# Kernel tuning notes

Hardware: AMD Instinct MI355X
Metric: run time of the kernel (lower is better)

Reference implementation:

```python
import jax, jax.numpy as jnp
import numpy as np

B = 131072          # batch (x in torch code; t=1, groups=1)
D = 128             # embedding_dim
K = 1024            # num_embeddings (codebook size)
COMMITMENT_COST = 0.25


def setup_inputs() -> dict:
    key = jax.random.key(0)
    k1, k2, k3 = jax.random.split(key, 3)
    inputs = jax.random.normal(k1, (B, D), dtype=jnp.float32)
    embedding = jax.random.normal(k2, (K, D), dtype=jnp.float32)
    # positive EMA cluster sizes (post-warmup state; torch init is zeros)
    ema_cluster_size = jax.random.uniform(k3, (K,), dtype=jnp.float32)
    return {"inputs": inputs, "embedding": embedding,
            "ema_cluster_size": ema_cluster_size}


def reference(inputs, embedding, ema_cluster_size):
    # groups=1, t=1: flat_input == inputs, shape [B, D]
    flat = inputs
    distances = (jnp.sum(flat * flat, axis=1, keepdims=True)
                 + jnp.sum(embedding * embedding, axis=1)
                 - 2.0 * jnp.matmul(flat, embedding.T))
    # module weights distances by EMA cluster size before argmin
    distances = distances * ema_cluster_size[None, :]
    encoding_indices = jnp.argmin(distances, axis=1)            # [B]
    # one-hot @ embedding == gather of codebook rows (same math, efficient)
    quantized = jnp.take(embedding, encoding_indices, axis=0)   # [B, D]
    # commitment loss: mse(stop_grad(quantized), inputs)
    e_latent_loss = jnp.mean((jax.lax.stop_gradient(quantized) - flat) ** 2)
    loss = COMMITMENT_COST * e_latent_loss
    # straight-through estimator
    quantized = flat + jax.lax.stop_gradient(quantized - flat)
    # z_embed: [bs, m] since t=1, groups=1; indices: [bs, groups] = [B, 1]
    z_embed = quantized
    return z_embed, loss, encoding_indices[:, None]
```

## Files before the change

kernel.cpp:

```cpp
#include <hip/hip_runtime.h>

#define DD   128
#define KTOT 1024
#define BTOT 131072

typedef __attribute__((ext_vector_type(8))) short bfrag8;
typedef __attribute__((ext_vector_type(16))) float facc16;

__device__ __forceinline__ unsigned short bf16_rne(float x) {
    unsigned u = __builtin_bit_cast(unsigned, x);
    u += 0x7fffu + ((u >> 16) & 1u);
    return (unsigned short)(u >> 16);
}
__device__ __forceinline__ float bf16f(unsigned short h) {
    unsigned u = ((unsigned)h) << 16;
    return __builtin_bit_cast(float, u);
}
__device__ __forceinline__ void gload_lds16(const void* g, void* l) {
    __builtin_amdgcn_global_load_lds(
        (const __attribute__((address_space(1))) void*)g,
        (__attribute__((address_space(3))) void*)l, 16, 0, 0);
}

__global__ __launch_bounds__(256) void vq_prep(
    const float* __restrict__ E, const float* __restrict__ ema,
    unsigned* __restrict__ Eh32, unsigned* __restrict__ El32,
    float* __restrict__ alpha, float* __restrict__ beta)
{
    const int tid = threadIdx.x, lane = tid & 63, wid = tid >> 6;
    const int k = blockIdx.x * 4 + wid;
    const float2 e2 = *(const float2*)(E + (size_t)k * DD + lane * 2);
    double ss = (double)e2.x * e2.x + (double)e2.y * e2.y;
    #pragma unroll
    for (int off = 1; off < 64; off <<= 1) ss += __shfl_xor(ss, off);
    float w = ema[k];
    float tw = -2.0f * w;
    float v0 = tw * e2.x, v1 = tw * e2.y;
    unsigned short h0 = bf16_rne(v0), h1 = bf16_rne(v1);
    unsigned short l0 = bf16_rne(v0 - bf16f(h0)), l1 = bf16_rne(v1 - bf16f(h1));
    Eh32[k * 64 + lane] = (unsigned)h0 | ((unsigned)h1 << 16);
    El32[k * 64 + lane] = (unsigned)l0 | ((unsigned)l1 << 16);
    if (lane == 0) { alpha[k] = w; beta[k] = (float)((double)w * ss); }
}

__global__ __launch_bounds__(256, 2) void vq_mfma(
    const float* __restrict__ X, const float* __restrict__ E,
    const unsigned short* __restrict__ Eh, const unsigned short* __restrict__ El,
    const float* __restrict__ alpha, const float* __restrict__ beta,
    float* __restrict__ outZ, float* __restrict__ outIdx,
    double* __restrict__ lossAcc, int* __restrict__ refCount,
    int* __restrict__ refList, int refCap)
{
    __shared__ __align__(1024) char smem[33280];
    int* ldsIdx = (int*)(smem + 32768);

    const int tid = threadIdx.x, lane = tid & 63, wid = tid >> 6;
    const int col = lane & 31, g2 = lane >> 5, m15 = lane & 15;
    const int rb = blockIdx.x * 128 + wid * 32;

    int soff[2], dofs[2];
    #pragma unroll
    for (int q = 0; q < 2; ++q) {
        int cb = wid * 8 + q * 4;
        int c = cb + (lane >> 4);
        soff[q] = c * 256 + ((m15 ^ (c & 15)) << 4);
        dofs[q] = cb * 256;
    }
    const char* EhB = (const char*)Eh;
    const char* ElB = (const char*)El;

    #pragma unroll
    for (int q = 0; q < 2; ++q) {
        gload_lds16(EhB + soff[q], smem + dofs[q]);
        gload_lds16(ElB + soff[q], smem + 8192 + dofs[q]);
    }

    bfrag8 Ah[8], Al[8];
    float p = 0.f;
    const float* xr = X + (size_t)(rb + col) * DD + g2 * 8;
    #pragma unroll
    for (int s = 0; s < 8; ++s) {
        float4 v0 = *(const float4*)(xr + s * 16);
        float4 v1 = *(const float4*)(xr + s * 16 + 4);
        float xs8[8] = {v0.x, v0.y, v0.z, v0.w, v1.x, v1.y, v1.z, v1.w};
        #pragma unroll
        for (int j = 0; j < 8; ++j) {
            float x = xs8[j];
            p = fmaf(x, x, p);
            unsigned short h = bf16_rne(x);
            Ah[s][j] = (short)h;
            Al[s][j] = (short)bf16_rne(x - bf16f(h));
        }
    }
    p += __shfl_xor(p, 32);
    float crs[16];
    #pragma unroll
    for (int r = 0; r < 16; ++r)
        crs[r] = __shfl(p, (r & 3) + 8 * (r >> 2) + 4 * g2);

    int rof[8];
    #pragma unroll
    for (int s = 0; s < 8; ++s)
        rof[s] = col * 256 + ((((s << 1) | g2) ^ m15) << 4);

    float b1[16], b2[16];
    int   i1[16];
    #pragma unroll
    for (int r = 0; r < 16; ++r) { b1[r] = 3e38f; b2[r] = 3e38f; i1[r] = 0; }

    __syncthreads();

    int cur = 0;
    #pragma unroll 2
    for (int t = 0; t < 32; ++t) {
        if (t + 1 < 32) {
            const char* eh2 = EhB + (size_t)(t + 1) * 8192;
            const char* el2 = ElB + (size_t)(t + 1) * 8192;
            char* nb = smem + ((cur ^ 1) * 16384);
            #pragma unroll
            for (int q = 0; q < 2; ++q) {
                gload_lds16(eh2 + soff[q], nb + dofs[q]);
                gload_lds16(el2 + soff[q], nb + 8192 + dofs[q]);
            }
        }
        const int cb32 = t * 32;
        float av = alpha[cb32 + col], bv = beta[cb32 + col];
        facc16 acc0, acc1;
        #pragma unroll
        for (int r = 0; r < 16; ++r) { acc0[r] = fmaf(av, crs[r], bv); acc1[r] = 0.f; }

        const char* bb = smem + cur * 16384;
        #pragma unroll
        for (int s = 0; s < 8; ++s) {
            bfrag8 Bh = *(const bfrag8*)(bb + rof[s]);
            bfrag8 Bl = *(const bfrag8*)(bb + 8192 + rof[s]);
            acc0 = __builtin_amdgcn_mfma_f32_32x32x16_bf16(Ah[s], Bh, acc0, 0, 0, 0);
            acc1 = __builtin_amdgcn_mfma_f32_32x32x16_bf16(Ah[s], Bl, acc1, 0, 0, 0);
            acc1 = __builtin_amdgcn_mfma_f32_32x32x16_bf16(Al[s], Bh, acc1, 0, 0, 0);
        }

        #pragma unroll
        for (int r = 0; r < 16; ++r) {
            float dd = acc0[r] + acc1[r];
            bool lt = dd < b1[r];
            b2[r] = fminf(b2[r], fmaxf(b1[r], dd));
            b1[r] = fminf(b1[r], dd);
            i1[r] = lt ? cb32 : i1[r];
        }
        __syncthreads();
        cur ^= 1;
    }

    int code[16];
    #pragma unroll
    for (int r = 0; r < 16; ++r) code[r] = i1[r] + col;
    #pragma unroll
    for (int off = 1; off < 32; off <<= 1) {
        #pragma unroll
        for (int r = 0; r < 16; ++r) {
            float ob1 = __shfl_xor(b1[r], off);
            float ob2 = __shfl_xor(b2[r], off);
            int   oc  = __shfl_xor(code[r], off);
            bool better = (ob1 < b1[r]) || (ob1 == b1[r] && oc < code[r]);
            float nb2 = better ? fminf(ob2, b1[r]) : fminf(b2[r], ob1);
            b1[r]   = better ? ob1 : b1[r];
            code[r] = better ? oc  : code[r];
            b2[r]   = nb2;
        }
    }

    double lsum = 0.0;
    if (col == 0) {
        #pragma unroll
        for (int r = 0; r < 16; ++r) {
            int rl = (r & 3) + 8 * (r >> 2) + 4 * g2;
            int row = rb + rl;
            int bc = code[r];
            outIdx[row] = (float)bc;
            ldsIdx[wid * 32 + rl] = bc;
            lsum += (double)b1[r] / (double)alpha[bc];
            float thr = fmaf(4e-4f, b1[r], 2e-6f);
            if (b2[r] - b1[r] < thr) {
                int pz = atomicAdd(refCount, 1);
                if (pz < refCap) refList[pz] = row;
            }
        }
    }
    lsum += __shfl_xor(lsum, 32);
    if (lane == 0) atomicAdd(lossAcc, lsum);

    __syncthreads();

    {
        int rl = lane >> 1;
        int best = ldsIdx[wid * 32 + rl];
        const float4* src = (const float4*)(E + (size_t)best * DD + (lane & 1) * 64);
        float4* dst = (float4*)(outZ + (size_t)(rb + rl) * DD + (lane & 1) * 64);
        #pragma unroll
        for (int q = 0; q < 16; ++q) dst[q] = src[q];
    }
}

__global__ void vq_refine(const float* __restrict__ X, const float* __restrict__ E,
                          const float* __restrict__ ema,
                          float* __restrict__ outZ, float* __restrict__ outIdx,
                          double* __restrict__ lossAcc,
                          const int* __restrict__ refCount,
                          const int* __restrict__ refList, int refCap)
{
    __shared__ float xs[DD];
    __shared__ double rb[256];
    __shared__ int    ri[256];
    __shared__ int    s_new, s_old;
    const int tid = threadIdx.x;
    int total = *refCount;
    if (total > refCap) total = refCap;

    for (int it = blockIdx.x; it < total; it += gridDim.x) {
        int row = refList[it];
        __syncthreads();
        if (tid < DD) xs[tid] = X[(size_t)row * DD + tid];
        __syncthreads();

        double lb = 1e300; int li = KTOT;
        #pragma unroll
        for (int j = 0; j < KTOT / 256; ++j) {
            int k = tid + j * 256;
            const float* e = E + (size_t)k * DD;
            double s = 0.0;
            for (int d = 0; d < DD; ++d) {
                double t = (double)xs[d] - (double)e[d];
                s = fma(t, t, s);
            }
            s *= (double)ema[k];
            if (s < lb) { lb = s; li = k; }
        }
        rb[tid] = lb; ri[tid] = li;
        __syncthreads();
        for (int st = 128; st > 0; st >>= 1) {
            if (tid < st) {
                double ob = rb[tid + st]; int oi = ri[tid + st];
                if (ob < rb[tid] || (ob == rb[tid] && oi < ri[tid])) { rb[tid] = ob; ri[tid] = oi; }
            }
            __syncthreads();
        }
        if (tid == 0) {
            int ni = ri[0];
            int oi = (int)outIdx[row];
            s_new = ni; s_old = oi;
            if (ni != oi) {
                const float* en = E + (size_t)ni * DD;
                const float* eo = E + (size_t)oi * DD;
                double dl = 0.0;
                for (int d = 0; d < DD; ++d) {
                    double dn  = (double)en[d] - (double)xs[d];
                    double dod = (double)eo[d] - (double)xs[d];
                    dl += dn * dn - dod * dod;
                }
                atomicAdd(lossAcc, dl);
                outIdx[row] = (float)ni;
            }
        }
        __syncthreads();
        if (s_new != s_old && tid < DD)
            outZ[(size_t)row * DD + tid] = E[(size_t)s_new * DD + tid];
    }
}

__global__ void vq_finalize(const double* __restrict__ lossAcc, float* __restrict__ outLoss) {
    *outLoss = (float)(0.25 * (*lossAcc) / ((double)BTOT * (double)DD));
}

extern "C" void kernel_launch(void* const* d_in, const int* in_sizes, int n_in,
                              void* d_out, int out_size, void* d_ws, size_t ws_size,
                              hipStream_t stream)
{
    const float* X   = (const float*)d_in[0];
    const float* E   = (const float*)d_in[1];
    const float* ema = (const float*)d_in[2];

    float* out     = (float*)d_out;
    float* outZ    = out;
    float* outLoss = out + (size_t)BTOT * DD;
    float* outIdx  = outLoss + 1;

    char* ws = (char*)d_ws;
    double* lossAcc = (double*)ws;
    int* refCount   = (int*)(ws + 8);
    float* alpha    = (float*)(ws + 16);
    float* beta     = (float*)(ws + 16 + 4096);
    unsigned short* Eh = (unsigned short*)(ws + 8208);
    unsigned short* El = (unsigned short*)(ws + 270352);
    int* refList    = (int*)(ws + 532496);
    long cap = ((long)ws_size - 532496) / 4;
    if (cap < 0) cap = 0;
    if (cap > BTOT) cap = BTOT;

    hipMemsetAsync(d_ws, 0, 16, stream);
    vq_prep<<<dim3(KTOT / 4), dim3(256), 0, stream>>>(
        E, ema, (unsigned*)Eh, (unsigned*)El, alpha, beta);
    vq_mfma<<<dim3(BTOT / 128), dim3(256), 0, stream>>>(
        X, E, Eh, El, alpha, beta, outZ, outIdx, lossAcc, refCount, refList, (int)cap);
    vq_refine<<<dim3(256), dim3(256), 0, stream>>>(
        X, E, ema, outZ, outIdx, lossAcc, refCount, refList, (int)cap);
    vq_finalize<<<dim3(1), dim3(1), 0, stream>>>(lossAcc, outLoss);
}
```

Measured before the change: 276.1 us.

## Triple-buffer codebook tiles with 512-thread blocks and LDS-cached alpha/beta

The main MFMA kernel now runs 512-thread blocks covering 256 rows, so each staged codebook tile is shared by twice as many waves. Codebook loads into LDS go through a three-stage ring with prefetch distance two. Explicit vmcnt waits and a single barrier per iteration replace the old double buffer, which needed two syncs per tile. Alpha and beta are copied into LDS once per block instead of being read from global memory each tile. The cost is more LDS per block (about 57KB) and register pressure under launch_bounds(512,4), which may limit occupancy or cause spills.

New measurement: 468.3 us. +69.6%, slower.

```diff
diff --git a/kernel.cpp b/kernel.cpp
--- a/kernel.cpp
+++ b/kernel.cpp
@@ -3,6 +3,7 @@
 #define DD   128
 #define KTOT 1024
 #define BTOT 131072
+#define NT   32
 
 typedef __attribute__((ext_vector_type(8))) short bfrag8;
 typedef __attribute__((ext_vector_type(16))) float facc16;
@@ -21,6 +22,7 @@
         (const __attribute__((address_space(1))) void*)g,
         (__attribute__((address_space(3))) void*)l, 16, 0, 0);
 }
+#define WAITV(N) asm volatile("s_waitcnt vmcnt(" #N ")" ::: "memory")
 
 __global__ __launch_bounds__(256) void vq_prep(
     const float* __restrict__ E, const float* __restrict__ ema,
@@ -43,7 +45,7 @@
     if (lane == 0) { alpha[k] = w; beta[k] = (float)((double)w * ss); }
 }
 
-__global__ __launch_bounds__(256, 2) void vq_mfma(
+__global__ __launch_bounds__(512, 4) void vq_mfma(
     const float* __restrict__ X, const float* __restrict__ E,
     const unsigned short* __restrict__ Eh, const unsigned short* __restrict__ El,
     const float* __restrict__ alpha, const float* __restrict__ beta,
@@ -51,28 +53,26 @@
     double* __restrict__ lossAcc, int* __restrict__ refCount,
     int* __restrict__ refList, int refCap)
 {
-    __shared__ __align__(1024) char smem[33280];
-    int* ldsIdx = (int*)(smem + 32768);
+    __shared__ __align__(1024) char smem[58368];
+    float* alphaLds = (float*)(smem + 49152);
+    float* betaLds  = (float*)(smem + 53248);
+    int*   ldsIdx   = (int*)(smem + 57344);
 
     const int tid = threadIdx.x, lane = tid & 63, wid = tid >> 6;
     const int col = lane & 31, g2 = lane >> 5, m15 = lane & 15;
-    const int rb = blockIdx.x * 128 + wid * 32;
-
-    int soff[2], dofs[2];
-    #pragma unroll
-    for (int q = 0; q < 2; ++q) {
-        int cb = wid * 8 + q * 4;
-        int c = cb + (lane >> 4);
-        soff[q] = c * 256 + ((m15 ^ (c & 15)) << 4);
-        dofs[q] = cb * 256;
-    }
+    const int rb = blockIdx.x * 256 + wid * 32;
+
+    const int c0 = tid >> 4;
+    const int soff = c0 * 256 + (((tid & 15) ^ (c0 & 15)) << 4);
     const char* EhB = (const char*)Eh;
     const char* ElB = (const char*)El;
-
-    #pragma unroll
-    for (int q = 0; q < 2; ++q) {
-        gload_lds16(EhB + soff[q], smem + dofs[q]);
-        gload_lds16(ElB + soff[q], smem + 8192 + dofs[q]);
+    char* const dstBase = smem + wid * 1024;
+
+    {
+        float2 a2 = *(const float2*)(alpha + tid * 2);
+        float2 b2v = *(const float2*)(beta + tid * 2);
+        *(float2*)(alphaLds + tid * 2) = a2;
+        *(float2*)(betaLds + tid * 2) = b2v;
     }
 
     bfrag8 Ah[8], Al[8];
@@ -108,28 +108,34 @@
     #pragma unroll
     for (int r = 0; r < 16; ++r) { b1[r] = 3e38f; b2[r] = 3e38f; i1[r] = 0; }
 
+    gload_lds16(EhB + soff, dstBase);
+    gload_lds16(ElB + soff, dstBase + 8192);
+    gload_lds16(EhB + 8192 + soff, dstBase + 16384);
+    gload_lds16(ElB + 8192 + soff, dstBase + 16384 + 8192);
     __syncthreads();
 
-    int cur = 0;
-    #pragma unroll 2
-    for (int t = 0; t < 32; ++t) {
-        if (t + 1 < 32) {
-            const char* eh2 = EhB + (size_t)(t + 1) * 8192;
-            const char* el2 = ElB + (size_t)(t + 1) * 8192;
-            char* nb = smem + ((cur ^ 1) * 16384);
-            #pragma unroll
-            for (int q = 0; q < 2; ++q) {
-                gload_lds16(eh2 + soff[q], nb + dofs[q]);
-                gload_lds16(el2 + soff[q], nb + 8192 + dofs[q]);
-            }
-        }
+    int bcur = 0;
+    for (int t = 0; t < NT; ++t) {
+        if (t + 1 < NT) { WAITV(2); } else { WAITV(0); }
+        __builtin_amdgcn_sched_barrier(0);
+        __builtin_amdgcn_s_barrier();
+
+        if (t + 2 < NT) {
+            int bst = bcur + 2; if (bst >= 3) bst -= 3;
+            const char* eh2 = EhB + (size_t)(t + 2) * 8192 + soff;
+            const char* el2 = ElB + (size_t)(t + 2) * 8192 + soff;
+            char* nb = dstBase + bst * 16384;
+            gload_lds16(eh2, nb);
+            gload_lds16(el2, nb + 8192);
+        }
+
         const int cb32 = t * 32;
-        float av = alpha[cb32 + col], bv = beta[cb32 + col];
+        float av = alphaLds[cb32 + col], bv = betaLds[cb32 + col];
         facc16 acc0, acc1;
         #pragma unroll
         for (int r = 0; r < 16; ++r) { acc0[r] = fmaf(av, crs[r], bv); acc1[r] = 0.f; }
 
-        const char* bb = smem + cur * 16384;
+        const char* bb = smem + bcur * 16384;
         #pragma unroll
         for (int s = 0; s < 8; ++s) {
             bfrag8 Bh = *(const bfrag8*)(bb + rof[s]);
@@ -147,8 +153,7 @@
             b1[r] = fminf(b1[r], dd);
             i1[r] = lt ? cb32 : i1[r];
         }
-        __syncthreads();
-        cur ^= 1;
+        bcur = (bcur == 2) ? 0 : bcur + 1;
     }
 
     int code[16];
@@ -169,6 +174,8 @@
         }
     }
 
+    __syncthreads();
+
     double lsum = 0.0;
     if (col == 0) {
         #pragma unroll
@@ -178,7 +185,7 @@
             int bc = code[r];
             outIdx[row] = (float)bc;
             ldsIdx[wid * 32 + rl] = bc;
-            lsum += (double)b1[r] / (double)alpha[bc];
+            lsum += (double)b1[r] / (double)alphaLds[bc];
             float thr = fmaf(4e-4f, b1[r], 2e-6f);
             if (b2[r] - b1[r] < thr) {
                 int pz = atomicAdd(refCount, 1);
@@ -299,7 +306,7 @@
     hipMemsetAsync(d_ws, 0, 16, stream);
     vq_prep<<<dim3(KTOT / 4), dim3(256), 0, stream>>>(
         E, ema, (unsigned*)Eh, (unsigned*)El, alpha, beta);
-    vq_mfma<<<dim3(BTOT / 128), dim3(256), 0, stream>>>(
+    vq_mfma<<<dim3(BTOT / 256), dim3(512), 0, stream>>>(
         X, E, Eh, El, alpha, beta, outZ, outIdx, lossAcc, refCount, refList, (int)cap);
     vq_refine<<<dim3(256), dim3(256), 0, stream>>>(
         X, E, ema, outZ, outIdx, lossAcc, refCount, refList, (int)cap);
```
